# Performance work log

Measured on AMD Instinct MI355X. Metric: run time of the kernel, lower is better.

## Reference

```python
import jax, jax.numpy as jnp
import numpy as np


def setup_inputs() -> dict:
    key = jax.random.key(0)
    k1, k2 = jax.random.split(key)
    B, N, D = 32, 1024, 512   # batch, patches per sample, d_model
    M = 4096                  # number of memory items
    queries = jax.random.normal(k1, (B, N, D), dtype=jnp.float32)
    items = jax.random.normal(k2, (M, D), dtype=jnp.float32)
    return {"queries": queries, "items": items}


def reference(queries, items):
    # queries: [B, N, D], items: [M, D]
    B, N, D = queries.shape
    q = queries.reshape(-1, D)                      # [B*N, D]
    score = jnp.matmul(q, items.T)                  # [B*N, M]
    # original: softmax(score) then top-1; softmax is monotone so
    # top-1 index of softmax == argmax of raw scores (same indices, same grads
    # since integer indices carry no gradient)
    idx = jnp.argmax(score, axis=1)                 # [B*N]
    gathered = items[idx]                           # [B*N, D]
    gathering_loss = (q - gathered) ** 2            # elementwise MSE (reduction='none')
    # reduce=True path: mean over all elements
    return jnp.mean(gathering_loss)
```

## Files before the change

kernel.cpp:

```cpp
#include <hip/hip_runtime.h>
#include <hip/hip_bf16.h>
#include <stdint.h>


#define D_DIM 512
#define M_ITEMS 4096
#define N_ROWS 32768
#define BM 128
#define GCOLS 512
#define NG (M_ITEMS / GCOLS)
#define APITCH 528

typedef _Float16 half8 __attribute__((ext_vector_type(8)));
typedef _Float16 half4h __attribute__((ext_vector_type(4)));
typedef float f32x16 __attribute__((ext_vector_type(16)));
typedef float f32x4v __attribute__((ext_vector_type(4)));
typedef int i32x8 __attribute__((ext_vector_type(8)));

__device__ inline unsigned pack4_fp8(float a, float b, float c, float d) {
  int v = 0;
  v = __builtin_amdgcn_cvt_pk_fp8_f32(a, b, v, false);
  v = __builtin_amdgcn_cvt_pk_fp8_f32(c, d, v, true);
  return (unsigned)v;
}

__global__ __launch_bounds__(256) void cast_f32_f16(
    const float* __restrict__ in, _Float16* __restrict__ out, int n4) {
  const int stride = gridDim.x * blockDim.x;
  for (int i = blockIdx.x * blockDim.x + threadIdx.x; i < n4; i += stride) {
    const f32x4v v = reinterpret_cast<const f32x4v*>(in)[i];
    half4h h;
    h.x = (_Float16)v.x;
    h.y = (_Float16)v.y;
    h.z = (_Float16)v.z;
    h.w = (_Float16)v.w;
    reinterpret_cast<half4h*>(out)[i] = h;
  }
}

__global__ __launch_bounds__(256) void pack_items_fp8(
    const float* __restrict__ itf, unsigned char* __restrict__ pk2) {
  const int u = blockIdx.x * blockDim.x + threadIdx.x;
  const int q = u & 3;
  const int c = (u >> 2) & 511;
  const int kc64 = (u >> 11) & 7;
  const int g = u >> 14;
  const int m = g * 512 + c;
  const float* src = itf + (size_t)m * D_DIM + kc64 * 64 + q * 16;
  const f32x4v a = *reinterpret_cast<const f32x4v*>(src);
  const f32x4v b = *reinterpret_cast<const f32x4v*>(src + 4);
  const f32x4v cc = *reinterpret_cast<const f32x4v*>(src + 8);
  const f32x4v d = *reinterpret_cast<const f32x4v*>(src + 12);
  uint4 o;
  o.x = pack4_fp8(a.x, a.y, a.z, a.w);
  o.y = pack4_fp8(b.x, b.y, b.z, b.w);
  o.z = pack4_fp8(cc.x, cc.y, cc.z, cc.w);
  o.w = pack4_fp8(d.x, d.y, d.z, d.w);
  *reinterpret_cast<uint4*>(pk2 + (size_t)u * 16) = o;
}

__global__ __launch_bounds__(512, 2) void score_mse(
    const float* __restrict__ qf, const unsigned char* __restrict__ pk2,
    const _Float16* __restrict__ ihl, float* __restrict__ partials) {
  __shared__ __align__(16) unsigned char Alds8[BM * APITCH];
  __shared__ float sV[4][BM];
  __shared__ int sI[4][BM];
  __shared__ float sSum[8];

  const int t = threadIdx.x;
  const int lane = t & 63;
  const int wid = t >> 6;
  const int wm = wid >> 2;
  const int wn = wid & 3;
  const int l31 = lane & 31;
  const int hsel = lane >> 5;

  const int bid = blockIdx.x;
  const int rb = (bid & 7) * 32 + (bid >> 3);
  const int row0 = rb * BM;

#pragma unroll
  for (int i = 0; i < 8; ++i) {
    const int f = i * 512 + t;
    const int r = f >> 5;
    const int u = f & 31;
    const float* src = qf + (size_t)(row0 + r) * D_DIM + u * 16;
    const f32x4v a = *(const f32x4v*)(src);
    const f32x4v b = *(const f32x4v*)(src + 4);
    const f32x4v c = *(const f32x4v*)(src + 8);
    const f32x4v d = *(const f32x4v*)(src + 12);
    uint4 o;
    o.x = pack4_fp8(a.x, a.y, a.z, a.w);
    o.y = pack4_fp8(b.x, b.y, b.z, b.w);
    o.z = pack4_fp8(c.x, c.y, c.z, c.w);
    o.w = pack4_fp8(d.x, d.y, d.z, d.w);
    *reinterpret_cast<uint4*>(Alds8 + (size_t)r * APITCH + u * 16) = o;
  }
  __syncthreads();

  f32x16 acc[2][4];
#pragma unroll
  for (int fr = 0; fr < 2; ++fr)
#pragma unroll
    for (int fc = 0; fc < 4; ++fc) acc[fr][fc] = (f32x16)(0.0f);
  float rmax[2][16];
  unsigned rid16[16];
#pragma unroll
  for (int rg = 0; rg < 16; ++rg) {
    rmax[0][rg] = -3.0e38f;
    rmax[1][rg] = -3.0e38f;
    rid16[rg] = 0u;
  }

  const unsigned char* Aptr0 =
      Alds8 + (size_t)(wm * 64 + l31) * APITCH + hsel * 32;
  const unsigned char* Aptr1 = Aptr0 + (size_t)32 * APITCH;
  const size_t bo0 = ((size_t)(wn * 128 + l31) << 6) + hsel * 32;

#pragma unroll 1
  for (int g = 0; g < NG; ++g) {
    const unsigned char* pgrp = pk2 + ((size_t)g << 18);
#pragma unroll 1
    for (int kc64 = 0; kc64 < 8; ++kc64) {
      const unsigned char* pchunk = pgrp + (kc64 << 15);
      const i32x8 av0 = *(const i32x8*)(Aptr0 + kc64 * 64);
      const i32x8 av1 = *(const i32x8*)(Aptr1 + kc64 * 64);
#pragma unroll
      for (int fc = 0; fc < 4; ++fc) {
        const i32x8 bv = *(const i32x8*)(pchunk + bo0 + fc * 2048);
        acc[0][fc] = __builtin_amdgcn_mfma_scale_f32_32x32x64_f8f6f4(
            av0, bv, acc[0][fc], 0, 0, 0, 127, 0, 127);
        acc[1][fc] = __builtin_amdgcn_mfma_scale_f32_32x32x64_f8f6f4(
            av1, bv, acc[1][fc], 0, 0, 0, 127, 0, 127);
      }
    }
    {
      const int colbase_ = g * GCOLS + wn * 128 + l31;
#pragma unroll
      for (int fr = 0; fr < 2; ++fr)
#pragma unroll
        for (int rg = 0; rg < 16; ++rg) {
          float v_ = acc[fr][0][rg];
          int c_ = colbase_;
#pragma unroll
          for (int fc = 1; fc < 4; ++fc) {
            const float vv_ = acc[fr][fc][rg];
            if (vv_ > v_) {
              v_ = vv_;
              c_ = colbase_ + fc * 32;
            }
          }
          if (v_ > rmax[fr][rg]) {
            rmax[fr][rg] = v_;
            rid16[rg] = (rid16[rg] & (fr ? 0x0000FFFFu : 0xFFFF0000u)) |
                        ((unsigned)c_ << (fr * 16));
          }
        }
#pragma unroll
      for (int fr = 0; fr < 2; ++fr)
#pragma unroll
        for (int fc = 0; fc < 4; ++fc) acc[fr][fc] = (f32x16)(0.0f);
    }
  }

  float bv = -3.0e38f;
  int bi = 0;
#pragma unroll
  for (int fr = 0; fr < 2; ++fr)
#pragma unroll
    for (int rg = 0; rg < 16; ++rg) {
      float v = rmax[fr][rg];
      int c = (int)((rid16[rg] >> (fr * 16)) & 0xFFFFu);
#pragma unroll
      for (int m = 1; m < 32; m <<= 1) {
        const float ov = __shfl_xor(v, m, 64);
        const int oc = __shfl_xor(c, m, 64);
        if (ov > v || (ov == v && oc < c)) {
          v = ov;
          c = oc;
        }
      }
      if (l31 == fr * 16 + rg) {
        bv = v;
        bi = c;
      }
    }
  const int e = l31;
  const int row_local =
      wm * 64 + (e >> 4) * 32 + ((e & 3) + 8 * ((e >> 2) & 3)) + 4 * hsel;

  sV[wn][row_local] = bv;
  sI[wn][row_local] = bi;
  __syncthreads();
  if (t < BM) {
    float fv = sV[0][t];
    int fi = sI[0][t];
#pragma unroll
    for (int w = 1; w < 4; ++w) {
      const float v = sV[w][t];
      const int ii = sI[w][t];
      if (v > fv || (v == fv && ii < fi)) {
        fv = v;
        fi = ii;
      }
    }
    sI[0][t] = fi;
  }
  __syncthreads();

  float lsum = 0.0f;
#pragma unroll 1
  for (int rr = 0; rr < 16; ++rr) {
    const int r = wid * 16 + rr;
    const int fi = sI[0][r];
    const float* qr = qf + (size_t)(row0 + r) * D_DIM + lane * 8;
    const f32x4v a0 = *(const f32x4v*)(qr);
    const f32x4v a1 = *(const f32x4v*)(qr + 4);
    const half8 ag = *(const half8*)(ihl + (size_t)fi * D_DIM + lane * 8);
    const float d0 = a0.x - (float)ag[0], d1 = a0.y - (float)ag[1];
    const float d2 = a0.z - (float)ag[2], d3 = a0.w - (float)ag[3];
    const float d4 = a1.x - (float)ag[4], d5 = a1.y - (float)ag[5];
    const float d6 = a1.z - (float)ag[6], d7 = a1.w - (float)ag[7];
    lsum += d0 * d0 + d1 * d1 + d2 * d2 + d3 * d3 + d4 * d4 + d5 * d5 +
            d6 * d6 + d7 * d7;
  }
#pragma unroll
  for (int m = 1; m < 64; m <<= 1) lsum += __shfl_xor(lsum, m, 64);
  if (lane == 0) sSum[wid] = lsum;
  __syncthreads();
  if (t == 0) {
    float s = 0.0f;
#pragma unroll
    for (int w = 0; w < 8; ++w) s += sSum[w];
    partials[bid] = s;
  }
}

__global__ __launch_bounds__(256) void final_reduce(
    const float* __restrict__ partials, float* __restrict__ out) {
  __shared__ float sS[4];
  const int t = threadIdx.x;
  float v = partials[t];
#pragma unroll
  for (int m = 1; m < 64; m <<= 1) v += __shfl_xor(v, m, 64);
  if ((t & 63) == 0) sS[t >> 6] = v;
  __syncthreads();
  if (t == 0)
    out[0] = (sS[0] + sS[1] + sS[2] + sS[3]) *
             (1.0f / ((float)N_ROWS * (float)D_DIM));
}

extern "C" void kernel_launch(void* const* d_in, const int* in_sizes, int n_in,
                              void* d_out, int out_size, void* d_ws,
                              size_t ws_size, hipStream_t stream) {
  const float* qf = (const float*)d_in[0];
  const float* itf = (const float*)d_in[1];
  char* ws = (char*)d_ws;
  unsigned char* pk2 = (unsigned char*)ws;
  _Float16* ihl = (_Float16*)(ws + (size_t)M_ITEMS * D_DIM);
  float* partials =
      (float*)(ws + (size_t)M_ITEMS * D_DIM + (size_t)M_ITEMS * D_DIM * 2);
  float* out = (float*)d_out;

  cast_f32_f16<<<512, 256, 0, stream>>>(itf, ihl, M_ITEMS * D_DIM / 4);
  pack_items_fp8<<<512, 256, 0, stream>>>(itf, pk2);
  score_mse<<<N_ROWS / BM, 512, 0, stream>>>(qf, pk2, ihl, partials);
  final_reduce<<<1, 256, 0, stream>>>(partials, out);
}
```

Baseline: 117.7 us.

## Software-pipeline fp8 MFMA loop with double-buffered register prefetch, halve accumulators

Flattens the group and K-chunk loops into one 128-step loop. Each step covers half of a group's columns, using a 2x2 accumulator tile instead of 2x4. The next step's A (LDS) and B (global) fragments are loaded into alternate register sets before the current MFMAs issue, so load latency can hide behind math. The trade-off is that the argmax epilogue runs twice as often and the A fragments are read from LDS twice as many times, in exchange for lower accumulator register pressure.

```diff
diff --git a/kernel.cpp b/kernel.cpp
--- a/kernel.cpp
+++ b/kernel.cpp
@@ -10,6 +10,7 @@
 #define GCOLS 512
 #define NG (M_ITEMS / GCOLS)
 #define APITCH 528
+#define NIT 128
 
 typedef _Float16 half8 __attribute__((ext_vector_type(8)));
 typedef _Float16 half4h __attribute__((ext_vector_type(4)));
@@ -98,11 +99,11 @@
   }
   __syncthreads();
 
-  f32x16 acc[2][4];
+  f32x16 acc[2][2];
 #pragma unroll
   for (int fr = 0; fr < 2; ++fr)
 #pragma unroll
-    for (int fc = 0; fc < 4; ++fc) acc[fr][fc] = (f32x16)(0.0f);
+    for (int fc = 0; fc < 2; ++fc) acc[fr][fc] = (f32x16)(0.0f);
   float rmax[2][16];
   unsigned rid16[16];
 #pragma unroll
@@ -115,52 +116,71 @@
   const unsigned char* Aptr0 =
       Alds8 + (size_t)(wm * 64 + l31) * APITCH + hsel * 32;
   const unsigned char* Aptr1 = Aptr0 + (size_t)32 * APITCH;
-  const size_t bo0 = ((size_t)(wn * 128 + l31) << 6) + hsel * 32;
-
+  const unsigned char* pB = pk2 + ((size_t)(wn * 128 + l31) << 6) + hsel * 32;
+
+#define BOFF(n)                                                                \
+  ((((size_t)((n) >> 4)) << 18) + (((size_t)((n) & 7)) << 15) +                \
+   (((size_t)(((n) >> 3) & 1)) << 12))
+
+#define LOADBV(n, B0, B1)                                                      \
+  do {                                                                         \
+    const unsigned char* p_ = pB + BOFF(n);                                    \
+    B0 = *(const i32x8*)(p_);                                                  \
+    B1 = *(const i32x8*)(p_ + 2048);                                           \
+  } while (0)
+
+#define LOADAV(n, A0, A1)                                                      \
+  do {                                                                         \
+    const int ko_ = ((n) & 7) * 64;                                            \
+    A0 = *(const i32x8*)(Aptr0 + ko_);                                         \
+    A1 = *(const i32x8*)(Aptr1 + ko_);                                         \
+  } while (0)
+
+#define PBODY(n, A0c, A1c, B0c, B1c, A0n, A1n, B0n, B1n)                       \
+  do {                                                                         \
+    if ((n) + 1 < NIT) {                                                       \
+      LOADBV((n) + 1, B0n, B1n);                                               \
+      LOADAV((n) + 1, A0n, A1n);                                               \
+    }                                                                          \
+    acc[0][0] = __builtin_amdgcn_mfma_scale_f32_32x32x64_f8f6f4(               \
+        A0c, B0c, acc[0][0], 0, 0, 0, 127, 0, 127);                            \
+    acc[0][1] = __builtin_amdgcn_mfma_scale_f32_32x32x64_f8f6f4(               \
+        A0c, B1c, acc[0][1], 0, 0, 0, 127, 0, 127);                            \
+    acc[1][0] = __builtin_amdgcn_mfma_scale_f32_32x32x64_f8f6f4(               \
+        A1c, B0c, acc[1][0], 0, 0, 0, 127, 0, 127);                            \
+    acc[1][1] = __builtin_amdgcn_mfma_scale_f32_32x32x64_f8f6f4(               \
+        A1c, B1c, acc[1][1], 0, 0, 0, 127, 0, 127);                            \
+    if (((n) & 7) == 7) {                                                      \
+      const int colbase_ =                                                     \
+          ((n) >> 4) * GCOLS + (((n) >> 3) & 1) * 64 + wn * 128 + l31;         \
+      _Pragma("unroll") for (int fr = 0; fr < 2; ++fr)                         \
+          _Pragma("unroll") for (int rg = 0; rg < 16; ++rg) {                  \
+        float v_ = acc[fr][0][rg];                                             \
+        int c_ = colbase_;                                                     \
+        const float vv_ = acc[fr][1][rg];                                      \
+        if (vv_ > v_) {                                                        \
+          v_ = vv_;                                                            \
+          c_ = colbase_ + 32;                                                  \
+        }                                                                      \
+        if (v_ > rmax[fr][rg]) {                                               \
+          rmax[fr][rg] = v_;                                                   \
+          rid16[rg] = (rid16[rg] & (fr ? 0x0000FFFFu : 0xFFFF0000u)) |         \
+                      ((unsigned)c_ << (fr * 16));                             \
+        }                                                                      \
+      }                                                                        \
+      _Pragma("unroll") for (int fr = 0; fr < 2; ++fr)                         \
+          _Pragma("unroll") for (int fc = 0; fc < 2; ++fc) acc[fr][fc] =       \
+              (f32x16)(0.0f);                                                  \
+    }                                                                          \
+  } while (0)
+
+  i32x8 avA0, avA1, avB0, avB1, bvA0, bvA1, bvB0, bvB1;
+  LOADBV(0, bvA0, bvA1);
+  LOADAV(0, avA0, avA1);
 #pragma unroll 1
-  for (int g = 0; g < NG; ++g) {
-    const unsigned char* pgrp = pk2 + ((size_t)g << 18);
-#pragma unroll 1
-    for (int kc64 = 0; kc64 < 8; ++kc64) {
-      const unsigned char* pchunk = pgrp + (kc64 << 15);
-      const i32x8 av0 = *(const i32x8*)(Aptr0 + kc64 * 64);
-      const i32x8 av1 = *(const i32x8*)(Aptr1 + kc64 * 64);
-#pragma unroll
-      for (int fc = 0; fc < 4; ++fc) {
-        const i32x8 bv = *(const i32x8*)(pchunk + bo0 + fc * 2048);
-        acc[0][fc] = __builtin_amdgcn_mfma_scale_f32_32x32x64_f8f6f4(
-            av0, bv, acc[0][fc], 0, 0, 0, 127, 0, 127);
-        acc[1][fc] = __builtin_amdgcn_mfma_scale_f32_32x32x64_f8f6f4(
-            av1, bv, acc[1][fc], 0, 0, 0, 127, 0, 127);
-      }
-    }
-    {
-      const int colbase_ = g * GCOLS + wn * 128 + l31;
-#pragma unroll
-      for (int fr = 0; fr < 2; ++fr)
-#pragma unroll
-        for (int rg = 0; rg < 16; ++rg) {
-          float v_ = acc[fr][0][rg];
-          int c_ = colbase_;
-#pragma unroll
-          for (int fc = 1; fc < 4; ++fc) {
-            const float vv_ = acc[fr][fc][rg];
-            if (vv_ > v_) {
-              v_ = vv_;
-              c_ = colbase_ + fc * 32;
-            }
-          }
-          if (v_ > rmax[fr][rg]) {
-            rmax[fr][rg] = v_;
-            rid16[rg] = (rid16[rg] & (fr ? 0x0000FFFFu : 0xFFFF0000u)) |
-                        ((unsigned)c_ << (fr * 16));
-          }
-        }
-#pragma unroll
-      for (int fr = 0; fr < 2; ++fr)
-#pragma unroll
-        for (int fc = 0; fc < 4; ++fc) acc[fr][fc] = (f32x16)(0.0f);
-    }
+  for (int n = 0; n < NIT; n += 2) {
+    PBODY(n, avA0, avA1, bvA0, bvA1, avB0, avB1, bvB0, bvB1);
+    PBODY(n + 1, avB0, avB1, bvB0, bvB1, avA0, avA1, bvA0, bvA1);
   }
 
   float bv = -3.0e38f;
```

After: 114.2 us. 2.9% less time.

## Halve row tile and per-wave accumulators to raise occupancy in FP8 score kernel

Applied to the files above, without the earlier changes.

Shrinks the row block from 128 to 64 rows and each wave's MFMA tile from 2x4 to 1x2 32x32 accumulators. The k-loop is flattened into a single 128-step loop with the argmax update every 8 steps. Launch bounds rise to 4 blocks per CU and the grid doubles to 512 blocks, with the final reduction reading two partials per thread. Lower register and LDS use should allow more concurrent waves to hide global B-load latency. The cost is less operand reuse per wave, so each block fetches B from global/L2 twice as often per row.

```diff
diff --git a/kernel.cpp b/kernel.cpp
--- a/kernel.cpp
+++ b/kernel.cpp
@@ -6,10 +6,11 @@
 #define D_DIM 512
 #define M_ITEMS 4096
 #define N_ROWS 32768
-#define BM 128
+#define BM 64
 #define GCOLS 512
 #define NG (M_ITEMS / GCOLS)
 #define APITCH 528
+#define NIT 128
 
 typedef _Float16 half8 __attribute__((ext_vector_type(8)));
 typedef _Float16 half4h __attribute__((ext_vector_type(4)));
@@ -59,7 +60,7 @@
   *reinterpret_cast<uint4*>(pk2 + (size_t)u * 16) = o;
 }
 
-__global__ __launch_bounds__(512, 2) void score_mse(
+__global__ __launch_bounds__(512, 4) void score_mse(
     const float* __restrict__ qf, const unsigned char* __restrict__ pk2,
     const _Float16* __restrict__ ihl, float* __restrict__ partials) {
   __shared__ __align__(16) unsigned char Alds8[BM * APITCH];
@@ -76,11 +77,11 @@
   const int hsel = lane >> 5;
 
   const int bid = blockIdx.x;
-  const int rb = (bid & 7) * 32 + (bid >> 3);
+  const int rb = (bid & 7) * 64 + (bid >> 3);
   const int row0 = rb * BM;
 
 #pragma unroll
-  for (int i = 0; i < 8; ++i) {
+  for (int i = 0; i < 4; ++i) {
     const int f = i * 512 + t;
     const int r = f >> 5;
     const int u = f & 31;
@@ -98,99 +99,75 @@
   }
   __syncthreads();
 
-  f32x16 acc[2][4];
-#pragma unroll
-  for (int fr = 0; fr < 2; ++fr)
-#pragma unroll
-    for (int fc = 0; fc < 4; ++fc) acc[fr][fc] = (f32x16)(0.0f);
-  float rmax[2][16];
-  unsigned rid16[16];
+  f32x16 acc[2];
+#pragma unroll
+  for (int fc = 0; fc < 2; ++fc) acc[fc] = (f32x16)(0.0f);
+  float rmax[16];
+  int rid[16];
 #pragma unroll
   for (int rg = 0; rg < 16; ++rg) {
-    rmax[0][rg] = -3.0e38f;
-    rmax[1][rg] = -3.0e38f;
-    rid16[rg] = 0u;
-  }
-
-  const unsigned char* Aptr0 =
-      Alds8 + (size_t)(wm * 64 + l31) * APITCH + hsel * 32;
-  const unsigned char* Aptr1 = Aptr0 + (size_t)32 * APITCH;
-  const size_t bo0 = ((size_t)(wn * 128 + l31) << 6) + hsel * 32;
+    rmax[rg] = -3.0e38f;
+    rid[rg] = 0;
+  }
+
+  const unsigned char* Aptr =
+      Alds8 + (size_t)(wm * 32 + l31) * APITCH + hsel * 32;
+  const unsigned char* pB = pk2 + ((size_t)(wn * 128 + l31) << 6) + hsel * 32;
 
 #pragma unroll 1
-  for (int g = 0; g < NG; ++g) {
-    const unsigned char* pgrp = pk2 + ((size_t)g << 18);
-#pragma unroll 1
-    for (int kc64 = 0; kc64 < 8; ++kc64) {
-      const unsigned char* pchunk = pgrp + (kc64 << 15);
-      const i32x8 av0 = *(const i32x8*)(Aptr0 + kc64 * 64);
-      const i32x8 av1 = *(const i32x8*)(Aptr1 + kc64 * 64);
-#pragma unroll
-      for (int fc = 0; fc < 4; ++fc) {
-        const i32x8 bv = *(const i32x8*)(pchunk + bo0 + fc * 2048);
-        acc[0][fc] = __builtin_amdgcn_mfma_scale_f32_32x32x64_f8f6f4(
-            av0, bv, acc[0][fc], 0, 0, 0, 127, 0, 127);
-        acc[1][fc] = __builtin_amdgcn_mfma_scale_f32_32x32x64_f8f6f4(
-            av1, bv, acc[1][fc], 0, 0, 0, 127, 0, 127);
-      }
-    }
-    {
-      const int colbase_ = g * GCOLS + wn * 128 + l31;
-#pragma unroll
-      for (int fr = 0; fr < 2; ++fr)
-#pragma unroll
-        for (int rg = 0; rg < 16; ++rg) {
-          float v_ = acc[fr][0][rg];
-          int c_ = colbase_;
-#pragma unroll
-          for (int fc = 1; fc < 4; ++fc) {
-            const float vv_ = acc[fr][fc][rg];
-            if (vv_ > v_) {
-              v_ = vv_;
-              c_ = colbase_ + fc * 32;
-            }
-          }
-          if (v_ > rmax[fr][rg]) {
-            rmax[fr][rg] = v_;
-            rid16[rg] = (rid16[rg] & (fr ? 0x0000FFFFu : 0xFFFF0000u)) |
-                        ((unsigned)c_ << (fr * 16));
-          }
+  for (int n = 0; n < NIT; ++n) {
+    const int g = n >> 4;
+    const int half = (n >> 3) & 1;
+    const int kc64 = n & 7;
+    const unsigned char* p_ =
+        pB + (((size_t)g << 18) + ((size_t)kc64 << 15) + ((size_t)half << 12));
+    const i32x8 bv0 = *(const i32x8*)(p_);
+    const i32x8 bv1 = *(const i32x8*)(p_ + 2048);
+    const i32x8 av = *(const i32x8*)(Aptr + kc64 * 64);
+    acc[0] = __builtin_amdgcn_mfma_scale_f32_32x32x64_f8f6f4(
+        av, bv0, acc[0], 0, 0, 0, 127, 0, 127);
+    acc[1] = __builtin_amdgcn_mfma_scale_f32_32x32x64_f8f6f4(
+        av, bv1, acc[1], 0, 0, 0, 127, 0, 127);
+    if ((n & 7) == 7) {
+      const int colbase = g * GCOLS + half * 64 + wn * 128 + l31;
+#pragma unroll
+      for (int rg = 0; rg < 16; ++rg) {
+        float v = acc[0][rg];
+        int c = colbase;
+        const float vv = acc[1][rg];
+        if (vv > v) {
+          v = vv;
+          c = colbase + 32;
         }
-#pragma unroll
-      for (int fr = 0; fr < 2; ++fr)
-#pragma unroll
-        for (int fc = 0; fc < 4; ++fc) acc[fr][fc] = (f32x16)(0.0f);
-    }
-  }
-
-  float bv = -3.0e38f;
-  int bi = 0;
-#pragma unroll
-  for (int fr = 0; fr < 2; ++fr)
-#pragma unroll
-    for (int rg = 0; rg < 16; ++rg) {
-      float v = rmax[fr][rg];
-      int c = (int)((rid16[rg] >> (fr * 16)) & 0xFFFFu);
-#pragma unroll
-      for (int m = 1; m < 32; m <<= 1) {
-        const float ov = __shfl_xor(v, m, 64);
-        const int oc = __shfl_xor(c, m, 64);
-        if (ov > v || (ov == v && oc < c)) {
-          v = ov;
-          c = oc;
+        if (v > rmax[rg]) {
+          rmax[rg] = v;
+          rid[rg] = c;
         }
       }
-      if (l31 == fr * 16 + rg) {
-        bv = v;
-        bi = c;
+#pragma unroll
+      for (int fc = 0; fc < 2; ++fc) acc[fc] = (f32x16)(0.0f);
+    }
+  }
+
+#pragma unroll
+  for (int rg = 0; rg < 16; ++rg) {
+    float v = rmax[rg];
+    int c = rid[rg];
+#pragma unroll
+    for (int m = 1; m < 32; m <<= 1) {
+      const float ov = __shfl_xor(v, m, 64);
+      const int oc = __shfl_xor(c, m, 64);
+      if (ov > v || (ov == v && oc < c)) {
+        v = ov;
+        c = oc;
       }
     }
-  const int e = l31;
-  const int row_local =
-      wm * 64 + (e >> 4) * 32 + ((e & 3) + 8 * ((e >> 2) & 3)) + 4 * hsel;
-
-  sV[wn][row_local] = bv;
-  sI[wn][row_local] = bi;
+    if (l31 == rg) {
+      const int row_local = wm * 32 + (rg & 3) + 8 * (rg >> 2) + 4 * hsel;
+      sV[wn][row_local] = v;
+      sI[wn][row_local] = c;
+    }
+  }
   __syncthreads();
   if (t < BM) {
     float fv = sV[0][t];
@@ -210,8 +187,8 @@
 
   float lsum = 0.0f;
 #pragma unroll 1
-  for (int rr = 0; rr < 16; ++rr) {
-    const int r = wid * 16 + rr;
+  for (int rr = 0; rr < 8; ++rr) {
+    const int r = wid * 8 + rr;
     const int fi = sI[0][r];
     const float* qr = qf + (size_t)(row0 + r) * D_DIM + lane * 8;
     const f32x4v a0 = *(const f32x4v*)(qr);
@@ -240,7 +217,7 @@
     const float* __restrict__ partials, float* __restrict__ out) {
   __shared__ float sS[4];
   const int t = threadIdx.x;
-  float v = partials[t];
+  float v = partials[t] + partials[t + 256];
 #pragma unroll
   for (int m = 1; m < 64; m <<= 1) v += __shfl_xor(v, m, 64);
   if ((t & 63) == 0) sS[t >> 6] = v;
```

After: 150.5 us. 27.9% more time.
